# Optimization experiments

Hardware: AMD Instinct MI355X
Metric: run time of the kernel (lower is better)

## Reference

```python
import jax, jax.numpy as jnp
import numpy as np

N_NODES = 10000
N_EDGES = 640000
HIDDEN = 128
OUT = 10

def setup_inputs() -> dict:
    key = jax.random.key(0)
    k1, k2, k3, k4 = jax.random.split(key, 4)
    x = jax.random.normal(k1, (N_NODES, HIDDEN), dtype=jnp.float32)
    edge_index = jax.random.randint(k2, (2, N_EDGES), 0, N_NODES, dtype=jnp.int64)
    # ClassifierMLP2 params: Linear(2*hidden -> hidden) -> ReLU -> Linear(hidden -> out)
    W1 = jax.random.normal(k3, (2 * HIDDEN, HIDDEN), dtype=jnp.float32) / np.sqrt(2 * HIDDEN)
    b1 = jnp.zeros((HIDDEN,), dtype=jnp.float32)
    W2 = jax.random.normal(k4, (HIDDEN, OUT), dtype=jnp.float32) / np.sqrt(HIDDEN)
    b2 = jnp.zeros((OUT,), dtype=jnp.float32)
    return {"x": x, "edge_index": edge_index, "W1": W1, "b1": b1, "W2": W2, "b2": b2}

def reference(x, edge_index, W1, b1, W2, b2):
    # mix_node_features(..., node_feat_mixing='cat'): gather src/dst node
    # embeddings per edge and concatenate along feature dim -> [E, 2*H]
    src, dst = edge_index[0], edge_index[1]
    edges_x = jnp.concatenate([x[src], x[dst]], axis=-1)  # [E, 2H]
    # ClassifierMLP2 (dropout inactive at inference)
    h = jax.nn.relu(edges_x @ W1 + b1)                    # [E, H]
    return h @ W2 + b2                                    # [E, OUT]
```

## Files before the change

kernel.cpp:

```cpp
#include <hip/hip_runtime.h>


typedef _Float16 f16;
typedef _Float16 f16x8 __attribute__((ext_vector_type(8)));
typedef float    f32x4 __attribute__((ext_vector_type(4)));

#define HID  128
#define TWOH 256
#define OUTD 10

__global__ __launch_bounds__(256) void w1_transpose(
    const float* __restrict__ W1,
    f16* __restrict__ W1T)
{
    const int idx = blockIdx.x * 256 + threadIdx.x;
    const int c = idx >> 7, k = idx & 127;
    const float v = (c < HID) ? W1[k * HID + c]
                              : W1[(HID + k) * HID + (c - HID)];
    W1T[idx] = (f16)v;
}

__global__ __launch_bounds__(256) void node_AB(
    const float* __restrict__ x,
    const f16* __restrict__ W1T,
    const float* __restrict__ b1,
    f16* __restrict__ AB,
    int n_nodes, int n_tiles)
{
    const int t = threadIdx.x;
    const int lane = t & 63;
    const int r = lane & 15, g = lane >> 4;
    const int wv = t >> 6;
    const int c0 = wv * 64;

    f16x8 w1f[4][4];
    float bias[4];
#pragma unroll
    for (int ct = 0; ct < 4; ++ct) {
        const int c = c0 + ct * 16 + r;
        bias[ct] = (c < HID) ? b1[c] : 0.f;
#pragma unroll
        for (int st = 0; st < 4; ++st)
            w1f[ct][st] = *(const f16x8*)(W1T + (long)c * HID + st * 32 + g * 8);
    }

    for (int tile = blockIdx.x; tile < n_tiles; tile += gridDim.x) {
        const int n0 = tile * 16;
        const int xrow = (n0 + r < n_nodes) ? (n0 + r) : (n_nodes - 1);

        f32x4 acc[4] = {{0,0,0,0},{0,0,0,0},{0,0,0,0},{0,0,0,0}};
#pragma unroll
        for (int st = 0; st < 4; ++st) {
            const float* xp = x + (long)xrow * HID + st * 32 + g * 8;
            const float4 x0 = *(const float4*)xp;
            const float4 x1 = *(const float4*)(xp + 4);
            f16x8 a;
            a[0] = (f16)x0.x; a[1] = (f16)x0.y; a[2] = (f16)x0.z; a[3] = (f16)x0.w;
            a[4] = (f16)x1.x; a[5] = (f16)x1.y; a[6] = (f16)x1.z; a[7] = (f16)x1.w;
#pragma unroll
            for (int ct = 0; ct < 4; ++ct)
                acc[ct] = __builtin_amdgcn_mfma_f32_16x16x32_f16(a, w1f[ct][st], acc[ct], 0, 0, 0);
        }

#pragma unroll
        for (int ct = 0; ct < 4; ++ct) {
            const int c = c0 + ct * 16 + r;
#pragma unroll
            for (int q = 0; q < 4; ++q) {
                const int node = n0 + g * 4 + q;
                if (node < n_nodes)
                    AB[(long)node * TWOH + c] = (f16)(acc[ct][q] + bias[ct]);
            }
        }
    }
}

__global__ __launch_bounds__(256) void edge_mlp(
    const f16* __restrict__ AB,
    const int* __restrict__ ei,
    const float* __restrict__ W2,
    const float* __restrict__ b2,
    float* __restrict__ out,
    int n_edges)
{
    __shared__ float stage[4][160];
    const int t = threadIdx.x;
    const int lane = t & 63;
    const int r = lane & 15, g = lane >> 4;
    const int wv = t >> 6;

    const bool cok = (r < OUTD);
    const int cw = cok ? r : 0;
    f16x8 w2f[4];
#pragma unroll
    for (int st = 0; st < 4; ++st) {
        f16x8 v;
#pragma unroll
        for (int j = 0; j < 8; ++j) {
            const float w = W2[(long)(st * 32 + g * 8 + j) * OUTD + cw];
            v[j] = cok ? (f16)w : (f16)0.f;
        }
        w2f[st] = v;
    }
    const float bj = cok ? b2[r] : 0.f;

    const f16x8* __restrict__ ABv = (const f16x8*)AB;
    const long eb = (long)blockIdx.x * 512 + wv * 128;

    int sn[8], dn[8];
#pragma unroll
    for (int it = 0; it < 8; ++it) {
        const long e = eb + it * 16 + r;
        const long ec = (e < n_edges) ? e : (n_edges - 1);
        sn[it] = ei[ec];
        dn[it] = ei[(long)n_edges + ec];
    }

    f16x8 pa[2][4], pc[2][4];
#pragma unroll
    for (int st = 0; st < 4; ++st) {
        pa[0][st] = ABv[(long)sn[0] * 32 + st * 4 + g];
        pc[0][st] = ABv[(long)dn[0] * 32 + 16 + st * 4 + g];
    }

#pragma unroll
    for (int it = 0; it < 8; ++it) {
        const int cur = it & 1, nxt = cur ^ 1;
        if (it < 7) {
            const long an = (long)sn[it + 1] * 32, bn = (long)dn[it + 1] * 32;
#pragma unroll
            for (int st = 0; st < 4; ++st) {
                pa[nxt][st] = ABv[an + st * 4 + g];
                pc[nxt][st] = ABv[bn + 16 + st * 4 + g];
            }
        }

        const f16x8 z = {0, 0, 0, 0, 0, 0, 0, 0};
        f32x4 acc = {0, 0, 0, 0};
#pragma unroll
        for (int st = 0; st < 4; ++st) {
            const f16x8 s = __builtin_elementwise_max(pa[cur][st] + pc[cur][st], z);
            acc = __builtin_amdgcn_mfma_f32_16x16x32_f16(s, w2f[st], acc, 0, 0, 0);
        }

        const long base = eb + (long)it * 16;
        if (base + 16 <= n_edges) {
            if (cok) {
#pragma unroll
                for (int q = 0; q < 4; ++q)
                    stage[wv][(g * 4 + q) * OUTD + r] = acc[q] + bj;
            }
            __builtin_amdgcn_wave_barrier();
            if (lane < 40) {
                const float4 vv = *(const float4*)&stage[wv][lane * 4];
                *(float4*)(out + base * OUTD + lane * 4) = vv;
            }
            __builtin_amdgcn_wave_barrier();
        } else if (cok) {
#pragma unroll
            for (int q = 0; q < 4; ++q) {
                const long ee = base + g * 4 + q;
                if (ee < n_edges) out[ee * OUTD + r] = acc[q] + bj;
            }
        }
    }
}

extern "C" void kernel_launch(void* const* d_in, const int* in_sizes, int n_in,
                              void* d_out, int out_size, void* d_ws, size_t ws_size,
                              hipStream_t stream) {
    const float* x  = (const float*)d_in[0];
    const int*   ei = (const int*)d_in[1];
    const float* W1 = (const float*)d_in[2];
    const float* b1 = (const float*)d_in[3];
    const float* W2 = (const float*)d_in[4];
    const float* b2 = (const float*)d_in[5];
    float* out = (float*)d_out;

    const int n_nodes = in_sizes[0] / HID;
    const int n_edges = in_sizes[1] / 2;
    const int n_tiles = (n_nodes + 15) / 16;

    f16* AB  = (f16*)d_ws;
    f16* W1T = AB + (long)n_nodes * TWOH;

    w1_transpose<<<(TWOH * HID) / 256, 256, 0, stream>>>(W1, W1T);

    int nb = (n_tiles + 1) / 2;
    node_AB<<<nb, 256, 0, stream>>>(x, W1T, b1, AB, n_nodes, n_tiles);

    edge_mlp<<<(n_edges + 511) / 512, 256, 0, stream>>>(AB, ei, W2, b2, out, n_edges);
}
```

Measured before the change: 66.58 us.

## Shrink per-block work in node and edge kernels to raise parallelism

node_AB now runs one 16-node tile per block with no grid-stride loop, and it issues the x loads before the W1 fragment loads. edge_mlp now processes 32 edges per wave instead of 128, which means 4x more blocks. Both gathers are issued up front, and results are written directly instead of staged through LDS. Launch bounds ask for 4 blocks per SM. The aim is more waves in flight to hide gather latency, at the cost of re-loading W1/W2 fragments per block and losing the coalesced float4 output stores.

New measurement: 81.67 us. 22.7% more time.

```diff
diff --git a/kernel.cpp b/kernel.cpp
--- a/kernel.cpp
+++ b/kernel.cpp
@@ -20,18 +20,28 @@
     W1T[idx] = (f16)v;
 }
 
-__global__ __launch_bounds__(256) void node_AB(
+__global__ __launch_bounds__(256, 4) void node_AB(
     const float* __restrict__ x,
     const f16* __restrict__ W1T,
     const float* __restrict__ b1,
     f16* __restrict__ AB,
-    int n_nodes, int n_tiles)
+    int n_nodes)
 {
     const int t = threadIdx.x;
     const int lane = t & 63;
     const int r = lane & 15, g = lane >> 4;
     const int wv = t >> 6;
     const int c0 = wv * 64;
+    const int n0 = blockIdx.x * 16;
+
+    const int xrow = (n0 + r < n_nodes) ? (n0 + r) : (n_nodes - 1);
+    float4 xl[4][2];
+#pragma unroll
+    for (int st = 0; st < 4; ++st) {
+        const float* xp = x + (long)xrow * HID + st * 32 + g * 8;
+        xl[st][0] = *(const float4*)xp;
+        xl[st][1] = *(const float4*)(xp + 4);
+    }
 
     f16x8 w1f[4][4];
     float bias[4];
@@ -44,38 +54,32 @@
             w1f[ct][st] = *(const f16x8*)(W1T + (long)c * HID + st * 32 + g * 8);
     }
 
-    for (int tile = blockIdx.x; tile < n_tiles; tile += gridDim.x) {
-        const int n0 = tile * 16;
-        const int xrow = (n0 + r < n_nodes) ? (n0 + r) : (n_nodes - 1);
-
-        f32x4 acc[4] = {{0,0,0,0},{0,0,0,0},{0,0,0,0},{0,0,0,0}};
+    f32x4 acc[4] = {{0,0,0,0},{0,0,0,0},{0,0,0,0},{0,0,0,0}};
 #pragma unroll
-        for (int st = 0; st < 4; ++st) {
-            const float* xp = x + (long)xrow * HID + st * 32 + g * 8;
-            const float4 x0 = *(const float4*)xp;
-            const float4 x1 = *(const float4*)(xp + 4);
-            f16x8 a;
-            a[0] = (f16)x0.x; a[1] = (f16)x0.y; a[2] = (f16)x0.z; a[3] = (f16)x0.w;
-            a[4] = (f16)x1.x; a[5] = (f16)x1.y; a[6] = (f16)x1.z; a[7] = (f16)x1.w;
+    for (int st = 0; st < 4; ++st) {
+        f16x8 a;
+        a[0] = (f16)xl[st][0].x; a[1] = (f16)xl[st][0].y;
+        a[2] = (f16)xl[st][0].z; a[3] = (f16)xl[st][0].w;
+        a[4] = (f16)xl[st][1].x; a[5] = (f16)xl[st][1].y;
+        a[6] = (f16)xl[st][1].z; a[7] = (f16)xl[st][1].w;
 #pragma unroll
-            for (int ct = 0; ct < 4; ++ct)
-                acc[ct] = __builtin_amdgcn_mfma_f32_16x16x32_f16(a, w1f[ct][st], acc[ct], 0, 0, 0);
-        }
+        for (int ct = 0; ct < 4; ++ct)
+            acc[ct] = __builtin_amdgcn_mfma_f32_16x16x32_f16(a, w1f[ct][st], acc[ct], 0, 0, 0);
+    }
 
 #pragma unroll
-        for (int ct = 0; ct < 4; ++ct) {
-            const int c = c0 + ct * 16 + r;
+    for (int ct = 0; ct < 4; ++ct) {
+        const int c = c0 + ct * 16 + r;
 #pragma unroll
-            for (int q = 0; q < 4; ++q) {
-                const int node = n0 + g * 4 + q;
-                if (node < n_nodes)
-                    AB[(long)node * TWOH + c] = (f16)(acc[ct][q] + bias[ct]);
-            }
+        for (int q = 0; q < 4; ++q) {
+            const int node = n0 + g * 4 + q;
+            if (node < n_nodes)
+                AB[(long)node * TWOH + c] = (f16)(acc[ct][q] + bias[ct]);
         }
     }
 }
 
-__global__ __launch_bounds__(256) void edge_mlp(
+__global__ __launch_bounds__(256, 4) void edge_mlp(
     const f16* __restrict__ AB,
     const int* __restrict__ ei,
     const float* __restrict__ W2,
@@ -83,7 +87,6 @@
     float* __restrict__ out,
     int n_edges)
 {
-    __shared__ float stage[4][160];
     const int t = threadIdx.x;
     const int lane = t & 63;
     const int r = lane & 15, g = lane >> 4;
@@ -105,63 +108,55 @@
     const float bj = cok ? b2[r] : 0.f;
 
     const f16x8* __restrict__ ABv = (const f16x8*)AB;
-    const long eb = (long)blockIdx.x * 512 + wv * 128;
+    const long eb = (long)blockIdx.x * 128 + wv * 32;
 
-    int sn[8], dn[8];
+    const long e0 = eb + r, e1 = eb + 16 + r;
+    const long c0i = (e0 < n_edges) ? e0 : (n_edges - 1);
+    const long c1i = (e1 < n_edges) ? e1 : (n_edges - 1);
+    const int sn0 = ei[c0i], dn0 = ei[(long)n_edges + c0i];
+    const int sn1 = ei[c1i], dn1 = ei[(long)n_edges + c1i];
+
+    const long a0 = (long)sn0 * 32, b0 = (long)dn0 * 32;
+    const long a1 = (long)sn1 * 32, b1 = (long)dn1 * 32;
+    f16x8 pa0[4], pc0[4], pa1[4], pc1[4];
 #pragma unroll
-    for (int it = 0; it < 8; ++it) {
-        const long e = eb + it * 16 + r;
-        const long ec = (e < n_edges) ? e : (n_edges - 1);
-        sn[it] = ei[ec];
-        dn[it] = ei[(long)n_edges + ec];
+    for (int st = 0; st < 4; ++st) {
+        pa0[st] = ABv[a0 + st * 4 + g];
+        pc0[st] = ABv[b0 + 16 + st * 4 + g];
+    }
+#pragma unroll
+    for (int st = 0; st < 4; ++st) {
+        pa1[st] = ABv[a1 + st * 4 + g];
+        pc1[st] = ABv[b1 + 16 + st * 4 + g];
     }
 
-    f16x8 pa[2][4], pc[2][4];
+    const f16x8 z = {0, 0, 0, 0, 0, 0, 0, 0};
+
+    f32x4 acc0 = {0, 0, 0, 0};
 #pragma unroll
     for (int st = 0; st < 4; ++st) {
-        pa[0][st] = ABv[(long)sn[0] * 32 + st * 4 + g];
-        pc[0][st] = ABv[(long)dn[0] * 32 + 16 + st * 4 + g];
+        const f16x8 s = __builtin_elementwise_max(pa0[st] + pc0[st], z);
+        acc0 = __builtin_amdgcn_mfma_f32_16x16x32_f16(s, w2f[st], acc0, 0, 0, 0);
+    }
+    if (cok) {
+#pragma unroll
+        for (int q = 0; q < 4; ++q) {
+            const long ee = eb + g * 4 + q;
+            if (ee < n_edges) out[ee * OUTD + r] = acc0[q] + bj;
+        }
     }
 
+    f32x4 acc1 = {0, 0, 0, 0};
 #pragma unroll
-    for (int it = 0; it < 8; ++it) {
-        const int cur = it & 1, nxt = cur ^ 1;
-        if (it < 7) {
-            const long an = (long)sn[it + 1] * 32, bn = (long)dn[it + 1] * 32;
+    for (int st = 0; st < 4; ++st) {
+        const f16x8 s = __builtin_elementwise_max(pa1[st] + pc1[st], z);
+        acc1 = __builtin_amdgcn_mfma_f32_16x16x32_f16(s, w2f[st], acc1, 0, 0, 0);
+    }
+    if (cok) {
 #pragma unroll
-            for (int st = 0; st < 4; ++st) {
-                pa[nxt][st] = ABv[an + st * 4 + g];
-                pc[nxt][st] = ABv[bn + 16 + st * 4 + g];
-            }
-        }
-
-        const f16x8 z = {0, 0, 0, 0, 0, 0, 0, 0};
-        f32x4 acc = {0, 0, 0, 0};
-#pragma unroll
-        for (int st = 0; st < 4; ++st) {
-            const f16x8 s = __builtin_elementwise_max(pa[cur][st] + pc[cur][st], z);
-            acc = __builtin_amdgcn_mfma_f32_16x16x32_f16(s, w2f[st], acc, 0, 0, 0);
-        }
-
-        const long base = eb + (long)it * 16;
-        if (base + 16 <= n_edges) {
-            if (cok) {
-#pragma unroll
-                for (int q = 0; q < 4; ++q)
-                    stage[wv][(g * 4 + q) * OUTD + r] = acc[q] + bj;
-            }
-            __builtin_amdgcn_wave_barrier();
-            if (lane < 40) {
-                const float4 vv = *(const float4*)&stage[wv][lane * 4];
-                *(float4*)(out + base * OUTD + lane * 4) = vv;
-            }
-            __builtin_amdgcn_wave_barrier();
-        } else if (cok) {
-#pragma unroll
-            for (int q = 0; q < 4; ++q) {
-                const long ee = base + g * 4 + q;
-                if (ee < n_edges) out[ee * OUTD + r] = acc[q] + bj;
-            }
+        for (int q = 0; q < 4; ++q) {
+            const long ee = eb + 16 + g * 4 + q;
+            if (ee < n_edges) out[ee * OUTD + r] = acc1[q] + bj;
         }
     }
 }
@@ -179,15 +174,13 @@
 
     const int n_nodes = in_sizes[0] / HID;
     const int n_edges = in_sizes[1] / 2;
-    const int n_tiles = (n_nodes + 15) / 16;
 
     f16* AB  = (f16*)d_ws;
     f16* W1T = AB + (long)n_nodes * TWOH;
 
     w1_transpose<<<(TWOH * HID) / 256, 256, 0, stream>>>(W1, W1T);
 
-    int nb = (n_tiles + 1) / 2;
-    node_AB<<<nb, 256, 0, stream>>>(x, W1T, b1, AB, n_nodes, n_tiles);
+    node_AB<<<(n_nodes + 15) / 16, 256, 0, stream>>>(x, W1T, b1, AB, n_nodes);
 
-    edge_mlp<<<(n_edges + 511) / 512, 256, 0, stream>>>(AB, ei, W2, b2, out, n_edges);
+    edge_mlp<<<(n_edges + 127) / 128, 256, 0, stream>>>(AB, ei, W2, b2, out, n_edges);
 }
```
